# Performance work log

Hardware: AMD Instinct MI355X
Metric: run time of the kernel (lower is better)

The kernel has to match this reference:

```python
import jax, jax.numpy as jnp
import numpy as np

PATCH = 16; EMBED = 768; HEADS = 12; DHEAD = 64
DEPTH_PRE = 2; DEPTH_SHORT = 8; PRIOR = 0.2
SCALE = 1.0 / float(DHEAD) ** 0.5
LN_EPS = 1e-5


def _ln(x, g, b):
    m = jnp.mean(x, -1, keepdims=True)
    v = jnp.mean(jnp.square(x - m), -1, keepdims=True)
    return (x - m) * jax.lax.rsqrt(v + LN_EPS) * g + b


def _pos_emb(T, d):
    # pos_seq = T-1 .. 0 (descending), sinusoidal [T, d]
    pos = jnp.arange(T - 1, -1, -1, dtype=jnp.float32)
    inv_freq = 1.0 / (10000.0 ** (jnp.arange(0.0, d, 2.0, dtype=jnp.float32) / d))
    s = pos[:, None] * inv_freq[None, :]
    return jnp.concatenate([jnp.sin(s), jnp.cos(s)], axis=-1)


def _rel_shift(x):
    # Transformer-XL relative shift: pad one zero col, reshape, drop first row
    b, h, q, r = x.shape
    xp = jnp.pad(x, ((0, 0), (0, 0), (0, 0), (1, 0)))
    return xp.reshape(b, h, r + 1, q)[:, :, 1:, :].reshape(b, h, q, r)


def _layer(x, r_emb, rwb, rrb, qkv_w, qkv_b, rn_w, rn_b, o_w, o_b,
           l1g, l1b, f1w, f1b, f2w, f2b, l2g, l2b):
    T, B, D = x.shape
    heads = x @ qkv_w.T + qkv_b
    q, k, v = jnp.split(heads, 3, axis=-1)
    q = q.reshape(T, B, HEADS, DHEAD)
    k = k.reshape(T, B, HEADS, DHEAD)
    v = v.reshape(T, B, HEADS, DHEAD)
    rk = (r_emb @ rn_w.T + rn_b).reshape(T, HEADS, DHEAD)
    AC = jnp.einsum('ibnd,jbnd->bnij', q + rwb, k)
    BD = _rel_shift(jnp.einsum('ibnd,jnd->bnij', q + rrb, rk))
    prob = jax.nn.softmax(SCALE * (AC + BD), axis=-1)  # no attn_mask in this model
    av = jnp.einsum('bnij,jbnd->ibnd', prob, v).reshape(T, B, D)
    x = _ln(x + av @ o_w.T + o_b, l1g, l1b)  # post-lnorm
    h = jax.nn.gelu(x @ f1w.T + f1b, approximate=False)
    return _ln(x + h @ f2w.T + f2b, l2g, l2b)


def setup_inputs() -> dict:
    key = jax.random.key(0)
    ks = jax.random.split(key, 16)
    f = jnp.float32
    D, H, FF, L = EMBED, HEADS, 3072, DEPTH_PRE + DEPTH_SHORT

    def w(k, shape, s=0.02):
        return jax.random.normal(k, shape, dtype=f) * s

    return {
        'x': jax.random.normal(ks[0], (32, 3, 224, 224), dtype=f),
        'patch_w': w(ks[1], (D, 3, PATCH, PATCH)),
        'patch_b': jnp.zeros((D,), f),
        'r_w_bias': jnp.zeros((H, DHEAD), f),
        'r_r_bias': jnp.zeros((H, DHEAD), f),
        'qkv_w': w(ks[2], (L, 3 * D, D)),
        'qkv_b': jnp.zeros((L, 3 * D), f),
        'rnet_w': w(ks[3], (L, D, D)),
        'rnet_b': jnp.zeros((L, D), f),
        'onet_w': w(ks[4], (L, D, D)),
        'onet_b': jnp.zeros((L, D), f),
        'ln1_g': jnp.ones((L, D), f), 'ln1_b': jnp.zeros((L, D), f),
        'ff1_w': w(ks[5], (L, FF, D)),
        'ff1_b': jnp.zeros((L, FF), f),
        'ff2_w': w(ks[6], (L, D, FF)),
        'ff2_b': jnp.zeros((L, D), f),
        'ln2_g': jnp.ones((L, D), f), 'ln2_b': jnp.zeros((L, D), f),
        'null_tok': w(ks[7], (1, 1, D)),
        'down_g': jnp.ones((D,), f), 'down_b': jnp.zeros((D,), f),
        'head_w': w(ks[8], (1000, D)),
        'head_b': jnp.zeros((1000,), f),
    }


def reference(x, patch_w, patch_b, r_w_bias, r_r_bias, qkv_w, qkv_b,
              rnet_w, rnet_b, onet_w, onet_b, ln1_g, ln1_b,
              ff1_w, ff1_b, ff2_w, ff2_b, ln2_g, ln2_b,
              null_tok, down_g, down_b, head_w, head_b):
    B = x.shape[0]
    # patch embed: conv stride=kernel=PATCH, NCHW
    h = jax.lax.conv_general_dilated(
        x, patch_w, (PATCH, PATCH), 'VALID',
        dimension_numbers=('NCHW', 'OIHW', 'NCHW')) + patch_b[None, :, None, None]
    T = h.shape[2] * h.shape[3]  # 196
    h = h.reshape(B, EMBED, T).transpose(2, 0, 1)  # [T, B, D]
    r = _pos_emb(T, EMBED)

    def blk(z, i, rr):
        return _layer(z, rr, r_w_bias, r_r_bias,
                      qkv_w[i], qkv_b[i], rnet_w[i], rnet_b[i],
                      onet_w[i], onet_b[i], ln1_g[i], ln1_b[i],
                      ff1_w[i], ff1_b[i], ff2_w[i], ff2_b[i],
                      ln2_g[i], ln2_b[i])

    for i in range(DEPTH_PRE):
        h = blk(h, i, r)

    # flop_measure boundaries: 1 every interval tokens; downsample = segment mean
    interval = max(1, int(1 / PRIOR))  # 5
    bnd = (jnp.arange(T) % interval == 0).astype(h.dtype)
    seg = (jnp.cumsum(bnd) - bnd).astype(jnp.int32)  # segment id per token
    S = int(np.ceil(T / interval))  # 40 (static)
    onehot = jax.nn.one_hot(seg, S, dtype=h.dtype)  # [T, S]
    pool = onehot / jnp.sum(onehot, axis=0, keepdims=True)
    short = jnp.einsum('tbd,ts->sbd', h, pool)  # [S, B, D]
    short = jnp.concatenate(
        [jnp.broadcast_to(null_tok.reshape(1, 1, EMBED), (1, B, EMBED)), short], axis=0)
    h = _ln(short, down_g, down_b)  # [S+1, B, D]

    r2 = _pos_emb(h.shape[0], EMBED)
    for i in range(DEPTH_PRE, DEPTH_PRE + DEPTH_SHORT):
        h = blk(h, i, r2)

    return h.mean(axis=0) @ head_w.T + head_b  # [B, 1000]
```

## Files before the change

### kernel.cpp

```cpp
#include <hip/hip_runtime.h>
#include <hip/hip_bf16.h>
#include <math.h>
#include <stdint.h>

typedef __bf16 bf16;
typedef __bf16 bf16x8 __attribute__((ext_vector_type(8)));
typedef float  f32x4  __attribute__((ext_vector_type(4)));

#define NB   32
#define ED   768
#define NH   12
#define DHD  64
#define FFD  3072
#define TT1  196
#define TT2  41
#define TPM  208
#define MM1  6272
#define MM2  1408
#define M2R  1312
#define BHN  384
#define LTOT 10
#define SCL  0.125f
#define VTS  224

__device__ __forceinline__ void gload_lds16(const bf16* g, bf16* l) {
  __builtin_amdgcn_global_load_lds(
      (__attribute__((address_space(1))) void*)(uintptr_t)g,
      (__attribute__((address_space(3))) void*)(uint32_t)(uintptr_t)l,
      16, 0, 0);
}

__device__ __forceinline__ float block_sum(float v, float* red, int tid) {
#pragma unroll
  for (int o = 32; o; o >>= 1) v += __shfl_xor(v, o);
  if ((tid & 63) == 0) red[tid >> 6] = v;
  __syncthreads();
  float t = red[0] + red[1] + red[2] + red[3];
  __syncthreads();
  return t;
}

__device__ __forceinline__ float gelu_f(float v) {
  const float u = v * (0.7978845608f + 0.0356774081f * v * v);
  const float t = 1.0f - 2.0f / (__expf(2.0f * u) + 1.0f);
  return 0.5f * v * (1.0f + t);
}

__device__ __forceinline__ bf16x8 cvt8(const float* __restrict__ s) {
  const f32x4 a = *(const f32x4*)s;
  const f32x4 b = *(const f32x4*)(s + 4);
  bf16x8 o;
#pragma unroll
  for (int j = 0; j < 4; ++j) { o[j] = (bf16)a[j]; o[4 + j] = (bf16)b[j]; }
  return o;
}

__global__ void k_cvt(const float* __restrict__ s, bf16* __restrict__ d, long n8) {
  for (long i = (long)blockIdx.x * 256 + threadIdx.x; i < n8; i += (long)gridDim.x * 256)
    *(bf16x8*)&d[i * 8] = cvt8(&s[i * 8]);
}

__global__ void k_cvt4(const float* __restrict__ a, const float* __restrict__ b,
                       const float* __restrict__ c, const float* __restrict__ d,
                       bf16* __restrict__ oa, bf16* __restrict__ ob,
                       bf16* __restrict__ oc, bf16* __restrict__ od,
                       int na8, int nb8, int nc8, int nd8) {
  const long tot = (long)na8 + nb8 + nc8 + nd8;
  for (long i = (long)blockIdx.x * 256 + threadIdx.x; i < tot; i += (long)gridDim.x * 256) {
    if (i < na8) *(bf16x8*)&oa[i * 8] = cvt8(&a[i * 8]);
    else if (i < (long)na8 + nb8) { const long j = i - na8; *(bf16x8*)&ob[j * 8] = cvt8(&b[j * 8]); }
    else if (i < (long)na8 + nb8 + nc8) { const long j = i - na8 - nb8; *(bf16x8*)&oc[j * 8] = cvt8(&c[j * 8]); }
    else { const long j = i - na8 - nb8 - nc8; *(bf16x8*)&od[j * 8] = cvt8(&d[j * 8]); }
  }
}

__global__ void k_posemb(bf16* __restrict__ out, int T) {
  const int t = blockIdx.x, c = threadIdx.x;
  float v = 0.0f;
  if (t < T) {
    const float pos = (float)(T - 1 - t);
    const int ci = (c < 384) ? c : c - 384;
    const float invf = expf(-(float)ci * (9.210340371976184f / 384.0f));
    const float a = pos * invf;
    v = (c < 384) ? sinf(a) : cosf(a);
  }
  out[(long)t * ED + c] = (bf16)v;
}

__global__ void k_im2col(const float* __restrict__ x, bf16* __restrict__ A0) {
  const long idx = (long)blockIdx.x * 256 + threadIdx.x;
  if (idx >= (long)MM1 * ED) return;
  const int row = (int)(idx / ED), k = (int)(idx % ED);
  const int t = row >> 5, b = row & 31;
  const int c = k >> 8, rem = k & 255, i = rem >> 4, j = rem & 15;
  const int py = t / 14, px = t % 14;
  A0[idx] = (bf16)x[((long)(b * 3 + c) * 224 + (py * 16 + i)) * 224 + px * 16 + j];
}

template <int EPI>
__global__ __launch_bounds__(256) void k_gemm(const bf16* __restrict__ A, const bf16* __restrict__ Bw,
                                              const float* __restrict__ bias,
                                              float* __restrict__ Cf, bf16* __restrict__ Cb,
                                              int M, int N, int K, int LDK) {
  __shared__ __align__(16) bf16 As[3][128 * 32];
  __shared__ __align__(16) bf16 Bs[3][128 * 32];
  const int tid = threadIdx.x;
  const int l = tid & 63, w = tid >> 6;
  const int wr = w >> 1, wc = w & 1;
  const int m0 = blockIdx.y * 128, n0 = blockIdx.x * 128;
  const long koff = (long)blockIdx.z * K;
  const int srow = l >> 2;
  const int scol = ((l & 3) ^ ((l >> 3) & 3)) * 8;
  f32x4 acc[4][4] = {};
  const int nt = K >> 5;

  auto stage = [&](int t, int b) {
    const int kt = t << 5;
#pragma unroll
    for (int p = 0; p < 2; ++p) {
      const int rbase = w * 32 + p * 16;
      gload_lds16(&A[(long)(m0 + rbase + srow) * LDK + koff + kt + scol], &As[b][rbase * 32]);
      gload_lds16(&Bw[(long)(n0 + rbase + srow) * LDK + koff + kt + scol], &Bs[b][rbase * 32]);
    }
  };

  stage(0, 0);
  stage(1, 1);

  int cur = 0;
  for (int t = 0; t < nt; ++t) {
    if (t + 2 < nt) {
      stage(t + 2, cur == 0 ? 2 : cur - 1);
      asm volatile("s_waitcnt vmcnt(8)" ::: "memory");
    } else if (t + 1 < nt) {
      asm volatile("s_waitcnt vmcnt(4)" ::: "memory");
    } else {
      asm volatile("s_waitcnt vmcnt(0)" ::: "memory");
    }
    __builtin_amdgcn_s_barrier();
    {
      bf16x8 af[4], bg[4];
      const int ub = l >> 4;
#pragma unroll
      for (int m = 0; m < 4; ++m) {
        const int row = wr * 64 + m * 16 + (l & 15);
        af[m] = *(const bf16x8*)&As[cur][row * 32 + (ub ^ ((row >> 1) & 3)) * 8];
      }
#pragma unroll
      for (int n = 0; n < 4; ++n) {
        const int row = wc * 64 + n * 16 + (l & 15);
        bg[n] = *(const bf16x8*)&Bs[cur][row * 32 + (ub ^ ((row >> 1) & 3)) * 8];
      }
#pragma unroll
      for (int m = 0; m < 4; ++m)
#pragma unroll
        for (int n = 0; n < 4; ++n)
          acc[m][n] = __builtin_amdgcn_mfma_f32_16x16x32_bf16(af[m], bg[n], acc[m][n], 0, 0, 0);
    }
    asm volatile("s_waitcnt lgkmcnt(0)" ::: "memory");
    __builtin_amdgcn_s_barrier();
    cur = (cur == 2) ? 0 : cur + 1;
  }

  const long pbase = (EPI == 4) ? (long)blockIdx.z * M * N : 0;
#pragma unroll
  for (int m = 0; m < 4; ++m) {
    const int row = m0 + wr * 64 + m * 16 + 4 * (l >> 4);
#pragma unroll
    for (int n = 0; n < 4; ++n) {
      const int col = n0 + wc * 64 + n * 16 + (l & 15);
      const float bv = (EPI == 4) ? 0.0f : bias[col];
#pragma unroll
      for (int r = 0; r < 4; ++r) {
        const float v = acc[m][n][r] + bv;
        const long off = (long)(row + r) * N + col;
        if (EPI == 0) {
          Cf[off] = v;
        } else if (EPI == 1) {
          Cb[off] = (bf16)gelu_f(v);
        } else if (EPI == 2) {
          Cf[off] = v;
          Cb[off] = (bf16)v;
        } else if (EPI == 3) {
          Cb[off] = (bf16)v;
        } else {
          Cf[pbase + off] = v;
        }
      }
    }
  }
}

__global__ __launch_bounds__(256) void k_redk_ln(const float* __restrict__ P, const float* __restrict__ bias,
                                                 const float* __restrict__ g, const float* __restrict__ bb,
                                                 const float* __restrict__ xin,
                                                 float* __restrict__ xo, bf16* __restrict__ xbo,
                                                 int KS, long MN, int Mreal) {
  const int row = blockIdx.x, tid = threadIdx.x;
  const long base = (long)row * ED;
  __shared__ float red[4];
  if (row >= Mreal) {
#pragma unroll
    for (int e = 0; e < 3; ++e) { xo[base + tid + e * 256] = 0.0f; xbo[base + tid + e * 256] = (bf16)0.0f; }
    return;
  }
  float v[3];
#pragma unroll
  for (int e = 0; e < 3; ++e) {
    const int c = tid + e * 256;
    float a = bias[c] + xin[base + c];
    for (int ks = 0; ks < KS; ++ks) a += P[(long)ks * MN + base + c];
    v[e] = a;
  }
  const float mean = block_sum(v[0] + v[1] + v[2], red, tid) * (1.0f / ED);
  float sq = 0.0f;
#pragma unroll
  for (int e = 0; e < 3; ++e) { const float dd = v[e] - mean; sq += dd * dd; }
  const float var = block_sum(sq, red, tid) * (1.0f / ED);
  const float rs = rsqrtf(var + 1e-5f);
#pragma unroll
  for (int e = 0; e < 3; ++e) {
    const int c = tid + e * 256;
    const float o = (v[e] - mean) * rs * g[c] + bb[c];
    xo[base + c] = o;
    xbo[base + c] = (bf16)o;
  }
}

__global__ __launch_bounds__(256) void k_vrepack(const bf16* __restrict__ heads, bf16* __restrict__ vT) {
  const int bh = blockIdx.x;
  const int b = bh / NH, n = bh % NH;
  const int tid = threadIdx.x;
  __shared__ __align__(16) bf16 vTl[64 * 232];
  for (int task = tid; task < 224 * 8; task += 256) {
    const int j = task >> 3, c8 = (task & 7) * 8;
    bf16x8 vv = {};
    if (j < TT1) vv = *(const bf16x8*)&heads[((long)(j * NB + b)) * (3 * ED) + 2 * ED + n * 64 + c8];
#pragma unroll
    for (int e = 0; e < 8; ++e) {
      const int d = c8 + e;
      vTl[d * 232 + (j ^ (((d >> 3) & 3) << 3))] = vv[e];
    }
  }
  __syncthreads();
  bf16* dst = vT + (long)bh * 64 * VTS;
  for (int task = tid; task < 64 * 28; task += 256) {
    const int d = task / 28, u = task % 28;
    const int j0 = u * 8;
    const int x = ((d >> 3) & 3) << 3;
    *(bf16x8*)&dst[d * VTS + j0] = *(const bf16x8*)&vTl[d * 232 + (j0 ^ x)];
  }
}

__global__ __launch_bounds__(256) void k_attn_pre(
    const bf16* __restrict__ heads, const float* __restrict__ rwb, const float* __restrict__ rrb,
    const bf16* __restrict__ rkb_l, const bf16* __restrict__ vT, bf16* __restrict__ avb) {
  const int r0 = blockIdx.x * 32;
  const int bh = blockIdx.y;
  const int b = bh / NH, n = bh % NH;
  const int tid = threadIdx.x;
  const int l = tid & 63, w = tid >> 6;
  const int fr = l & 15;
  const int fc = 8 * (l >> 4);
  __shared__ float Sl[32 * 209];
  __shared__ __align__(16) bf16 probl[32 * 232];
  __shared__ float red8[256];
  __shared__ float rstat[32];

  {
    const int ti = w & 1;
    const int ar = r0 + ti * 16 + fr;
    bf16x8 qa0 = {}, qa1 = {};
    if (ar < TT1) {
      const bf16* qp = &heads[((long)(ar * NB + b)) * (3 * ED) + n * 64];
      qa0 = *(const bf16x8*)(qp + fc);
      qa1 = *(const bf16x8*)(qp + 32 + fc);
    }
    bf16x8 q0, q1;
#pragma unroll
    for (int e = 0; e < 8; ++e) {
      q0[e] = (bf16)((float)qa0[e] + rwb[n * 64 + fc + e]);
      q1[e] = (bf16)((float)qa1[e] + rwb[n * 64 + 32 + fc + e]);
    }
    auto ldk = [&](int tj, bf16x8& k0, bf16x8& k1) {
      const int br = tj * 16 + fr;
      k0 = bf16x8{}; k1 = bf16x8{};
      if (br < TT1) {
        const bf16* kp = &heads[((long)(br * NB + b)) * (3 * ED) + ED + n * 64];
        k0 = *(const bf16x8*)(kp + fc);
        k1 = *(const bf16x8*)(kp + 32 + fc);
      }
    };
    bf16x8 k0, k1, nk0, nk1;
    const int tj0 = w >> 1;
    ldk(tj0, k0, k1);
    for (int tj = tj0; tj < 13; tj += 2) {
      if (tj + 2 < 13) ldk(tj + 2, nk0, nk1);
      f32x4 c = {};
      c = __builtin_amdgcn_mfma_f32_16x16x32_bf16(q0, k0, c, 0, 0, 0);
      c = __builtin_amdgcn_mfma_f32_16x16x32_bf16(q1, k1, c, 0, 0, 0);
      const int scol = tj * 16 + fr;
      const int srb = ti * 16 + 4 * (l >> 4);
#pragma unroll
      for (int r = 0; r < 4; ++r) Sl[(srb + r) * 209 + scol] = SCL * c[r];
      k0 = nk0; k1 = nk1;
    }
  }
  __syncthreads();

  {
    bf16x8 qr0[3], qr1[3];
#pragma unroll
    for (int ta = 0; ta < 3; ++ta) {
      const int ar = r0 + ta * 16 + fr;
      bf16x8 qa0 = {}, qa1 = {};
      if (ar < TT1) {
        const bf16* qp = &heads[((long)(ar * NB + b)) * (3 * ED) + n * 64];
        qa0 = *(const bf16x8*)(qp + fc);
        qa1 = *(const bf16x8*)(qp + 32 + fc);
      }
#pragma unroll
      for (int e = 0; e < 8; ++e) {
        qr0[ta][e] = (bf16)((float)qa0[e] + rrb[n * 64 + fc + e]);
        qr1[ta][e] = (bf16)((float)qa1[e] + rrb[n * 64 + 32 + fc + e]);
      }
    }
    auto ldr = [&](int tb, bf16x8& g0, bf16x8& g1) {
      const int br = tb * 16 + fr;
      const bf16* rp = &rkb_l[((long)n * TPM + br) * 64];
      g0 = *(const bf16x8*)(rp + fc);
      g1 = *(const bf16x8*)(rp + 32 + fc);
    };
    bf16x8 g0, g1, ng0, ng1;
    if (w < 13) ldr(w, g0, g1);
    for (int tb = w; tb < 13; tb += 4) {
      if (tb + 4 < 13) ldr(tb + 4, ng0, ng1);
#pragma unroll
      for (int ta = 0; ta < 3; ++ta) {
        f32x4 c = {};
        c = __builtin_amdgcn_mfma_f32_16x16x32_bf16(qr0[ta], g0, c, 0, 0, 0);
        c = __builtin_amdgcn_mfma_f32_16x16x32_bf16(qr1[ta], g1, c, 0, 0, 0);
        const int bcol = tb * 16 + fr;
        const int ab = r0 + ta * 16 + 4 * (l >> 4);
#pragma unroll
        for (int r = 0; r < 4; ++r) {
          const int a = ab + r;
          if (a < TT1 && bcol < TT1) {
            const int m = a * (TT1 + 1) + bcol + 1;
            if (m >= TT1) {
              const int i = m / TT1 - 1;
              const int j = m - (i + 1) * TT1;
              const int li = i - r0;
              if (li >= 0 && li < 32) Sl[li * 209 + j] += SCL * c[r];
            }
          }
        }
      }
      g0 = ng0; g1 = ng1;
    }
  }
  __syncthreads();

  const int sr = tid & 31, sg = tid >> 5;
  const bool rowok = (r0 + sr) < TT1;
  const int j0 = sg * 25;
  const int j1 = (j0 + 25 < TT1) ? j0 + 25 : TT1;
  float pm = -3.0e38f;
  if (rowok) {
    for (int j = j0; j < j1; ++j) pm = fmaxf(pm, Sl[sr * 209 + j]);
  }
  red8[sr * 8 + sg] = pm;
  __syncthreads();
  if (tid < 32) {
    float m0 = red8[tid * 8];
#pragma unroll
    for (int q = 1; q < 8; ++q) m0 = fmaxf(m0, red8[tid * 8 + q]);
    rstat[tid] = m0;
  }
  __syncthreads();
  const float rm = rstat[sr];
  float ps = 0.0f;
  if (rowok) {
    for (int j = j0; j < j1; ++j) {
      const float e = __expf(Sl[sr * 209 + j] - rm);
      Sl[sr * 209 + j] = e;
      ps += e;
    }
  }
  red8[sr * 8 + sg] = ps;
  __syncthreads();
  if (tid < 32) {
    float s0 = 0.0f;
#pragma unroll
    for (int q = 0; q < 8; ++q) s0 += red8[tid * 8 + q];
    rstat[tid] = (s0 > 0.0f) ? 1.0f / s0 : 0.0f;
  }
  __syncthreads();
  const float inv = rstat[sr];
  const int sx = ((sr >> 3) & 3) << 3;
  for (int j = sg * 28; j < sg * 28 + 28; ++j) {
    const float v = (rowok && j < TT1) ? Sl[sr * 209 + j] * inv : 0.0f;
    probl[sr * 232 + (j ^ sx)] = (bf16)v;
  }
  __syncthreads();

  const bf16* vTg = vT + (long)bh * 64 * VTS;
  for (int tt = w; tt < 8; tt += 4) {
    const int ti = tt & 1, dj = tt >> 1;
    const int prow = ti * 16 + fr;
    const int vrow = dj * 16 + fr;
    const int px = ((prow >> 3) & 3) << 3;
    f32x4 c = {};
#pragma unroll
    for (int kk = 0; kk < 224; kk += 32) {
      const int j0v = kk + fc;
      const bf16x8 pa = *(const bf16x8*)&probl[prow * 232 + (j0v ^ px)];
      const bf16x8 vb = *(const bf16x8*)&vTg[vrow * VTS + j0v];
      c = __builtin_amdgcn_mfma_f32_16x16x32_bf16(pa, vb, c, 0, 0, 0);
    }
    const int d = dj * 16 + fr;
    const int ib = ti * 16 + 4 * (l >> 4);
#pragma unroll
    for (int r = 0; r < 4; ++r) {
      const int gi = r0 + ib + r;
      if (gi < TT1) avb[((long)(gi * NB + b)) * ED + n * 64 + d] = (bf16)c[r];
    }
  }
}

__global__ __launch_bounds__(256) void k_attn_short(
    const bf16* __restrict__ heads, const float* __restrict__ rwb, const float* __restrict__ rrb,
    const bf16* __restrict__ rkb_l, bf16* __restrict__ avb) {
  const int bh = blockIdx.x;
  const int b = bh / NH, n = bh % NH;
  const int tid = threadIdx.x;
  const int l = tid & 63, w = tid >> 6;
  const int fr = l & 15, fc = 8 * (l >> 4);
  __shared__ float Sl[48 * 49];
  __shared__ __align__(16) bf16 probl[48 * 72];
  __shared__ __align__(16) bf16 vTl[64 * 72];

  for (int task = tid; task < 64 * 8; task += 256) {
    const int j = task >> 3, c8 = (task & 7) * 8;
    bf16x8 vv = {};
    if (j < TT2) vv = *(const bf16x8*)&heads[((long)(j * NB + b)) * (3 * ED) + 2 * ED + n * 64 + c8];
#pragma unroll
    for (int e = 0; e < 8; ++e) {
      const int d = c8 + e;
      vTl[d * 72 + (j ^ (((d >> 3) & 3) << 3))] = vv[e];
    }
  }

  for (int tt = w; tt < 9; tt += 4) {
    const int ti = tt / 3, tj = tt % 3;
    const int ar = ti * 16 + fr;
    const int br = tj * 16 + fr;
    f32x4 c = {};
#pragma unroll
    for (int kk = 0; kk < 64; kk += 32) {
      const int col = kk + fc;
      bf16x8 qa = {}, kb = {};
      if (ar < 44) qa = *(const bf16x8*)&heads[((long)(ar * NB + b)) * (3 * ED) + n * 64 + col];
      if (br < 44) kb = *(const bf16x8*)&heads[((long)(br * NB + b)) * (3 * ED) + ED + n * 64 + col];
      bf16x8 qq;
#pragma unroll
      for (int e = 0; e < 8; ++e) qq[e] = (bf16)((float)qa[e] + rwb[n * 64 + col + e]);
      c = __builtin_amdgcn_mfma_f32_16x16x32_bf16(qq, kb, c, 0, 0, 0);
    }
    const int scol = tj * 16 + fr;
    const int srb = ti * 16 + 4 * (l >> 4);
#pragma unroll
    for (int r = 0; r < 4; ++r) Sl[(srb + r) * 49 + scol] = SCL * c[r];
  }
  __syncthreads();

  for (int tt = w; tt < 9; tt += 4) {
    const int ti = tt / 3, tj = tt % 3;
    const int ar = ti * 16 + fr;
    const int br = tj * 16 + fr;
    f32x4 c = {};
#pragma unroll
    for (int kk = 0; kk < 64; kk += 32) {
      const int col = kk + fc;
      bf16x8 qa = {};
      if (ar < 44) qa = *(const bf16x8*)&heads[((long)(ar * NB + b)) * (3 * ED) + n * 64 + col];
      const bf16x8 rk = *(const bf16x8*)&rkb_l[((long)n * TPM + br) * 64 + col];
      bf16x8 qq;
#pragma unroll
      for (int e = 0; e < 8; ++e) qq[e] = (bf16)((float)qa[e] + rrb[n * 64 + col + e]);
      c = __builtin_amdgcn_mfma_f32_16x16x32_bf16(qq, rk, c, 0, 0, 0);
    }
    const int bcol = tj * 16 + fr;
    const int ab = ti * 16 + 4 * (l >> 4);
#pragma unroll
    for (int r = 0; r < 4; ++r) {
      const int a = ab + r;
      if (a < TT2 && bcol < TT2) {
        const int m = a * (TT2 + 1) + bcol + 1;
        if (m >= TT2) {
          const int i = m / TT2 - 1;
          const int j = m - (i + 1) * TT2;
          Sl[i * 49 + j] += SCL * c[r];
        }
      }
    }
  }
  __syncthreads();

  if (tid < 48) {
    const int i = tid;
    const int ix = ((i >> 3) & 3) << 3;
    if (i < TT2) {
      float mx = -3.0e38f;
      for (int j = 0; j < TT2; ++j) mx = fmaxf(mx, Sl[i * 49 + j]);
      float sm = 0.0f;
      for (int j = 0; j < TT2; ++j) { const float e = expf(Sl[i * 49 + j] - mx); Sl[i * 49 + j] = e; sm += e; }
      const float inv = 1.0f / sm;
      for (int j = 0; j < TT2; ++j) probl[i * 72 + (j ^ ix)] = (bf16)(Sl[i * 49 + j] * inv);
      for (int j = TT2; j < 64; ++j) probl[i * 72 + (j ^ ix)] = (bf16)0.0f;
    } else {
      for (int j = 0; j < 64; ++j) probl[i * 72 + (j ^ ix)] = (bf16)0.0f;
    }
  }
  __syncthreads();

  for (int tt = w; tt < 12; tt += 4) {
    const int ti = tt % 3, dj = tt / 3;
    const int prow = ti * 16 + fr;
    const int vrow = dj * 16 + fr;
    const int px = ((prow >> 3) & 3) << 3;
    const int vx = ((vrow >> 3) & 3) << 3;
    f32x4 c = {};
#pragma unroll
    for (int kk = 0; kk < 64; kk += 32) {
      const int j0 = kk + fc;
      const bf16x8 pa = *(const bf16x8*)&probl[prow * 72 + (j0 ^ px)];
      const bf16x8 vb = *(const bf16x8*)&vTl[vrow * 72 + (j0 ^ vx)];
      c = __builtin_amdgcn_mfma_f32_16x16x32_bf16(pa, vb, c, 0, 0, 0);
    }
    const int d = dj * 16 + fr;
    const int ib = ti * 16 + 4 * (l >> 4);
#pragma unroll
    for (int r = 0; r < 4; ++r) {
      const int i = ib + r;
      if (i < TT2) avb[((long)(i * NB + b)) * ED + n * 64 + d] = (bf16)c[r];
    }
  }
}

__global__ void k_rkrepack(const float* __restrict__ rkall, bf16* __restrict__ rkb,
                           int T, int Ncols, int l0) {
  const int i = blockIdx.x, z = blockIdx.y, d = threadIdx.x;
  const float v = (i < T) ? rkall[(long)i * Ncols + z * ED + d] : 0.0f;
  const int n = d >> 6, dh = d & 63;
  rkb[(((long)(l0 + z) * NH + n) * TPM + i) * 64 + dh] = (bf16)v;
}

__global__ __launch_bounds__(256) void k_ln(const float* __restrict__ xin, const float* __restrict__ add,
                                            const float* __restrict__ g, const float* __restrict__ bb,
                                            float* __restrict__ xo, bf16* __restrict__ xbo, int Mreal) {
  const int row = blockIdx.x, tid = threadIdx.x;
  const long base = (long)row * ED;
  __shared__ float red[4];
  if (row >= Mreal) {
#pragma unroll
    for (int e = 0; e < 3; ++e) { xo[base + tid + e * 256] = 0.0f; xbo[base + tid + e * 256] = (bf16)0.0f; }
    return;
  }
  float v[3];
#pragma unroll
  for (int e = 0; e < 3; ++e) v[e] = xin[base + tid + e * 256] + add[base + tid + e * 256];
  const float mean = block_sum(v[0] + v[1] + v[2], red, tid) * (1.0f / ED);
  float sq = 0.0f;
#pragma unroll
  for (int e = 0; e < 3; ++e) { const float dd = v[e] - mean; sq += dd * dd; }
  const float var = block_sum(sq, red, tid) * (1.0f / ED);
  const float rs = rsqrtf(var + 1e-5f);
#pragma unroll
  for (int e = 0; e < 3; ++e) {
    const int c = tid + e * 256;
    const float o = (v[e] - mean) * rs * g[c] + bb[c];
    xo[base + c] = o;
    xbo[base + c] = (bf16)o;
  }
}

__global__ __launch_bounds__(256) void k_down(const float* __restrict__ x, const float* __restrict__ nullt,
                                              const float* __restrict__ g, const float* __restrict__ bb,
                                              float* __restrict__ xo, bf16* __restrict__ xbo) {
  const int row = blockIdx.x, tid = threadIdx.x;
  const long base = (long)row * ED;
  __shared__ float red[4];
  if (row >= TT2 * NB) {
#pragma unroll
    for (int e = 0; e < 3; ++e) { xo[base + tid + e * 256] = 0.0f; xbo[base + tid + e * 256] = (bf16)0.0f; }
    return;
  }
  const int s = row >> 5, b = row & 31;
  float v[3];
  if (s == 0) {
#pragma unroll
    for (int e = 0; e < 3; ++e) v[e] = nullt[tid + e * 256];
  } else {
    const int seg = s - 1;
    const int t0 = (seg == 0) ? 0 : (5 * seg - 4);
    const int cnt = (seg == 0) ? 1 : 5;
#pragma unroll
    for (int e = 0; e < 3; ++e) {
      float a = 0.0f;
      for (int tt = 0; tt < cnt; ++tt) a += x[((long)((t0 + tt) * NB + b)) * ED + tid + e * 256];
      v[e] = a / (float)cnt;
    }
  }
  const float mean = block_sum(v[0] + v[1] + v[2], red, tid) * (1.0f / ED);
  float sq = 0.0f;
#pragma unroll
  for (int e = 0; e < 3; ++e) { const float dd = v[e] - mean; sq += dd * dd; }
  const float var = block_sum(sq, red, tid) * (1.0f / ED);
  const float rs = rsqrtf(var + 1e-5f);
#pragma unroll
  for (int e = 0; e < 3; ++e) {
    const int c = tid + e * 256;
    const float o = (v[e] - mean) * rs * g[c] + bb[c];
    xo[base + c] = o;
    xbo[base + c] = (bf16)o;
  }
}

__global__ __launch_bounds__(256) void k_mean(const float* __restrict__ x2, float* __restrict__ xm) {
  const int b = blockIdx.x, tid = threadIdx.x;
#pragma unroll
  for (int e = 0; e < 3; ++e) {
    const int c = tid + e * 256;
    float a = 0.0f;
    for (int s = 0; s < TT2; ++s) a += x2[((long)(s * NB + b)) * ED + c];
    xm[(long)b * ED + c] = a * (1.0f / TT2);
  }
}

__global__ __launch_bounds__(256) void k_head(const float* __restrict__ xm, const float* __restrict__ hw,
                                              const float* __restrict__ hbias, float* __restrict__ out) {
  const int gid = blockIdx.x * 4 + (threadIdx.x >> 6);
  const int l = threadIdx.x & 63;
  if (gid >= NB * 1000) return;
  const int b = gid / 1000, n = gid % 1000;
  const float* xr = xm + (long)b * ED;
  const float* wr = hw + (long)n * ED;
  float a = 0.0f;
#pragma unroll
  for (int e = 0; e < 12; ++e) a += xr[l + 64 * e] * wr[l + 64 * e];
#pragma unroll
  for (int o = 32; o; o >>= 1) a += __shfl_xor(a, o);
  if (l == 0) out[(long)b * 1000 + n] = a + hbias[n];
}

extern "C" void kernel_launch(void* const* d_in, const int* in_sizes, int n_in,
                              void* d_out, int out_size, void* d_ws, size_t ws_size,
                              hipStream_t stream) {
  const float* in_x     = (const float*)d_in[0];
  const float* patch_w  = (const float*)d_in[1];
  const float* patch_b  = (const float*)d_in[2];
  const float* r_w_bias = (const float*)d_in[3];
  const float* r_r_bias = (const float*)d_in[4];
  const float* qkv_w    = (const float*)d_in[5];
  const float* qkv_b    = (const float*)d_in[6];
  const float* rnet_w   = (const float*)d_in[7];
  const float* rnet_b   = (const float*)d_in[8];
  const float* onet_w   = (const float*)d_in[9];
  const float* onet_b   = (const float*)d_in[10];
  const float* ln1_g    = (const float*)d_in[11];
  const float* ln1_b    = (const float*)d_in[12];
  const float* ff1_w    = (const float*)d_in[13];
  const float* ff1_b    = (const float*)d_in[14];
  const float* ff2_w    = (const float*)d_in[15];
  const float* ff2_b    = (const float*)d_in[16];
  const float* ln2_g    = (const float*)d_in[17];
  const float* ln2_b    = (const float*)d_in[18];
  const float* null_tok = (const float*)d_in[19];
  const float* down_g   = (const float*)d_in[20];
  const float* down_b   = (const float*)d_in[21];
  const float* head_w   = (const float*)d_in[22];
  const float* head_b   = (const float*)d_in[23];
  float* out = (float*)d_out;

  char* base = (char*)d_ws;
  size_t off = 0;
  auto take = [&](size_t bytes) -> char* {
    char* r = base + off;
    off += (bytes + 255) & ~(size_t)255;
    return r;
  };

  float* x    = (float*)take((size_t)MM1 * ED * 4);
  bf16*  xb   = (bf16*)take((size_t)MM1 * ED * 2);
  float* x2   = (float*)take((size_t)MM2 * ED * 4);
  bf16*  xb2  = (bf16*)take((size_t)MM2 * ED * 2);
  bf16*  rkb  = (bf16*)take((size_t)LTOT * NH * TPM * 64 * 2);
  bf16*  rbf  = (bf16*)take((size_t)256 * ED * 2);
  bf16*  r2bf = (bf16*)take((size_t)128 * ED * 2);
  float* xm   = (float*)take((size_t)NB * ED * 4);

  char* arenaW = take((size_t)(2304 * 768 + 768 * 768 + 3072 * 768 + 768 * 3072) * 2);
  bf16* wq = (bf16*)arenaW;
  bf16* wo = wq + (size_t)2304 * 768;
  bf16* w1 = wo + (size_t)768 * 768;
  bf16* w2 = w1 + (size_t)3072 * 768;
  bf16* wrnet  = (bf16*)arenaW;
  bf16* wpatch = wrnet + (size_t)LTOT * 768 * 768;

  char* arenaQ = take((size_t)MM1 * ED * 2 + (size_t)4 * MM2 * ED * 4);
  bf16*  A0 = (bf16*)arenaQ;
  bf16*  vT = (bf16*)arenaQ;
  float* P  = (float*)arenaQ;

  char* arenaH = take((size_t)MM1 * 3 * ED * 2);
  bf16*  headsb = (bf16*)arenaH;
  float* rkall1 = (float*)arenaH;
  float* rkall2 = (float*)(arenaH + (size_t)256 * 1536 * 4);

  char* arenaS = take((size_t)MM1 * ED * 2 + (size_t)MM1 * ED * 4 + (size_t)MM1 * FFD * 2);
  bf16*  avb  = (bf16*)arenaS;
  float* gout = (float*)(arenaS + (size_t)MM1 * ED * 2);
  bf16*  hb   = (bf16*)(arenaS + (size_t)MM1 * ED * 2 + (size_t)MM1 * ED * 4);

  if (off > ws_size) return;

  k_posemb<<<dim3(256), dim3(768), 0, stream>>>(rbf, TT1);
  k_posemb<<<dim3(128), dim3(768), 0, stream>>>(r2bf, TT2);
  k_cvt<<<dim3(1024), dim3(256), 0, stream>>>(rnet_w, wrnet, (long)LTOT * 768 * 768 / 8);
  k_cvt<<<dim3(288), dim3(256), 0, stream>>>(patch_w, wpatch, (long)768 * 768 / 8);
  k_im2col<<<dim3((MM1 * ED + 255) / 256), dim3(256), 0, stream>>>(in_x, A0);
  k_gemm<2><<<dim3(6, 49, 1), dim3(256), 0, stream>>>(A0, wpatch, patch_b, x, xb, MM1, ED, ED, ED);
  k_gemm<0><<<dim3(12, 2, 1), dim3(256), 0, stream>>>(rbf, wrnet, rnet_b, rkall1, nullptr, 256, 1536, ED, ED);
  k_gemm<0><<<dim3(48, 1, 1), dim3(256), 0, stream>>>(r2bf, wrnet + (size_t)2 * 768 * 768, rnet_b + 2 * 768,
                                                      rkall2, nullptr, 128, 6144, ED, ED);
  k_rkrepack<<<dim3(TPM, 2), dim3(768), 0, stream>>>(rkall1, rkb, TT1, 1536, 0);
  k_rkrepack<<<dim3(48, 8), dim3(768), 0, stream>>>(rkall2, rkb, TT2, 6144, 2);

  for (int l = 0; l < LTOT; ++l) {
    const bool pre = (l < 2);
    const int Mp = pre ? MM1 : MM2;
    const int Mreal = pre ? MM1 : M2R;
    float* xcur = pre ? x : x2;
    bf16* xbcur = pre ? xb : xb2;

    k_cvt4<<<dim3(1024), dim3(256), 0, stream>>>(
        qkv_w + (size_t)l * 2304 * 768, onet_w + (size_t)l * 768 * 768,
        ff1_w + (size_t)l * 3072 * 768, ff2_w + (size_t)l * 768 * 3072,
        wq, wo, w1, w2, 2304 * 768 / 8, 768 * 768 / 8, 3072 * 768 / 8, 768 * 3072 / 8);

    k_gemm<3><<<dim3(18, Mp / 128, 1), dim3(256), 0, stream>>>(xbcur, wq, qkv_b + (size_t)l * 2304,
                                                               nullptr, headsb, Mp, 3 * ED, ED, ED);
    if (pre) {
      k_vrepack<<<dim3(BHN), dim3(256), 0, stream>>>(headsb, vT);
      k_attn_pre<<<dim3(7, BHN), dim3(256), 0, stream>>>(
          headsb, r_w_bias, r_r_bias, rkb + (size_t)l * NH * TPM * 64, vT, avb);
      k_gemm<0><<<dim3(6, Mp / 128, 1), dim3(256), 0, stream>>>(avb, wo, onet_b + (size_t)l * 768,
                                                                gout, nullptr, Mp, ED, ED, ED);
      k_ln<<<dim3(Mp), dim3(256), 0, stream>>>(xcur, gout, ln1_g + (size_t)l * 768, ln1_b + (size_t)l * 768,
                                               xcur, xbcur, Mreal);
      k_gemm<1><<<dim3(24, Mp / 128, 1), dim3(256), 0, stream>>>(xbcur, w1, ff1_b + (size_t)l * 3072,
                                                                 nullptr, hb, Mp, FFD, ED, ED);
      k_gemm<0><<<dim3(6, Mp / 128, 1), dim3(256), 0, stream>>>(hb, w2, ff2_b + (size_t)l * 768,
                                                                gout, nullptr, Mp, ED, FFD, FFD);
      k_ln<<<dim3(Mp), dim3(256), 0, stream>>>(xcur, gout, ln2_g + (size_t)l * 768, ln2_b + (size_t)l * 768,
                                               xcur, xbcur, Mreal);
    } else {
      k_attn_short<<<dim3(BHN), dim3(256), 0, stream>>>(
          headsb, r_w_bias, r_r_bias, rkb + (size_t)l * NH * TPM * 64, avb);
      k_gemm<4><<<dim3(6, Mp / 128, 2), dim3(256), 0, stream>>>(avb, wo, nullptr,
                                                                P, nullptr, Mp, ED, 384, ED);
      k_redk_ln<<<dim3(Mp), dim3(256), 0, stream>>>(P, onet_b + (size_t)l * 768,
                                                    ln1_g + (size_t)l * 768, ln1_b + (size_t)l * 768,
                                                    xcur, xcur, xbcur, 2, (long)Mp * ED, Mreal);
      k_gemm<1><<<dim3(24, Mp / 128, 1), dim3(256), 0, stream>>>(xbcur, w1, ff1_b + (size_t)l * 3072,
                                                                 nullptr, hb, Mp, FFD, ED, ED);
      k_gemm<4><<<dim3(6, Mp / 128, 4), dim3(256), 0, stream>>>(hb, w2, nullptr,
                                                                P, nullptr, Mp, ED, 768, FFD);
      k_redk_ln<<<dim3(Mp), dim3(256), 0, stream>>>(P, ff2_b + (size_t)l * 768,
                                                    ln2_g + (size_t)l * 768, ln2_b + (size_t)l * 768,
                                                    xcur, xcur, xbcur, 4, (long)Mp * ED, Mreal);
    }

    if (l == 1) {
      k_down<<<dim3(MM2), dim3(256), 0, stream>>>(x, null_tok, down_g, down_b, x2, xb2);
    }
  }

  k_mean<<<dim3(NB), dim3(256), 0, stream>>>(x2, xm);
  k_head<<<dim3(8000), dim3(256), 0, stream>>>(xm, head_w, head_b, out);
}
```

Measured before the change: 1.447 ms.

## Read fp32 weights directly in short-stage GEMMs, remap blocks across XCDs

For the eight short-sequence layers, the GEMM now streams fp32 weights straight into LDS and converts them to bf16 at fragment-load time. This removes the per-layer k_cvt4 conversion kernel, along with its extra write and re-read of the weights. The cost is twice the weight bytes per tile, larger LDS use, and conversion ALU work in the inner loop. All GEMMs also get a block-index remap so that consecutive tiles land on the same XCD, which is meant to improve L2 locality.

```diff
diff --git a/kernel.cpp b/kernel.cpp
--- a/kernel.cpp
+++ b/kernel.cpp
@@ -23,7 +23,7 @@
 #define SCL  0.125f
 #define VTS  224
 
-__device__ __forceinline__ void gload_lds16(const bf16* g, bf16* l) {
+__device__ __forceinline__ void gload_lds16(const void* g, void* l) {
   __builtin_amdgcn_global_load_lds(
       (__attribute__((address_space(1))) void*)(uintptr_t)g,
       (__attribute__((address_space(3))) void*)(uint32_t)(uintptr_t)l,
@@ -97,20 +97,34 @@
   A0[idx] = (bf16)x[((long)(b * 3 + c) * 224 + (py * 16 + i)) * 224 + px * 16 + j];
 }
 
-template <int EPI>
+template <int EPI, int BF32>
 __global__ __launch_bounds__(256) void k_gemm(const bf16* __restrict__ A, const bf16* __restrict__ Bw,
+                                              const float* __restrict__ Bw32,
                                               const float* __restrict__ bias,
                                               float* __restrict__ Cf, bf16* __restrict__ Cb,
                                               int M, int N, int K, int LDK) {
-  __shared__ __align__(16) bf16 As[3][128 * 32];
-  __shared__ __align__(16) bf16 Bs[3][128 * 32];
+  constexpr int BELEM = 128 * 32;
+  __shared__ __align__(16) bf16 As[3][BELEM];
+  constexpr int BBYTES = BF32 ? 3 * BELEM * 4 : 3 * BELEM * 2;
+  __shared__ __align__(16) char Braw[BBYTES];
   const int tid = threadIdx.x;
   const int l = tid & 63, w = tid >> 6;
   const int wr = w >> 1, wc = w & 1;
-  const int m0 = blockIdx.y * 128, n0 = blockIdx.x * 128;
+
+  const int gx = gridDim.x, gy = gridDim.y;
+  int flat = blockIdx.x * gy + blockIdx.y;
+  const int nwg = gx * gy;
+  const int xcd = flat & 7, idx = flat >> 3;
+  const int qq = nwg >> 3, rr = nwg & 7;
+  flat = (xcd < rr ? xcd * (qq + 1) : rr * (qq + 1) + (xcd - rr) * qq) + idx;
+  const int bx = flat / gy;
+  const int m0 = (flat - bx * gy) * 128, n0 = bx * 128;
+
   const long koff = (long)blockIdx.z * K;
-  const int srow = l >> 2;
-  const int scol = ((l & 3) ^ ((l >> 3) & 3)) * 8;
+  const int srowA = l >> 2;
+  const int scolA = ((l & 3) ^ ((l >> 3) & 3)) * 8;
+  const int srowB = l >> 3;
+  const int scolB = ((l & 7) ^ (((l >> 3) & 3) << 1)) * 4;
   f32x4 acc[4][4] = {};
   const int nt = K >> 5;
 
@@ -119,8 +133,22 @@
 #pragma unroll
     for (int p = 0; p < 2; ++p) {
       const int rbase = w * 32 + p * 16;
-      gload_lds16(&A[(long)(m0 + rbase + srow) * LDK + koff + kt + scol], &As[b][rbase * 32]);
-      gload_lds16(&Bw[(long)(n0 + rbase + srow) * LDK + koff + kt + scol], &Bs[b][rbase * 32]);
+      gload_lds16(&A[(long)(m0 + rbase + srowA) * LDK + koff + kt + scolA], &As[b][rbase * 32]);
+    }
+    if constexpr (BF32) {
+      float* Bb = (float*)Braw + (long)b * BELEM;
+#pragma unroll
+      for (int p = 0; p < 4; ++p) {
+        const int rbase = w * 32 + p * 8;
+        gload_lds16(&Bw32[(long)(n0 + rbase + srowB) * LDK + koff + kt + scolB], &Bb[rbase * 32]);
+      }
+    } else {
+      bf16* Bb = (bf16*)Braw + (long)b * BELEM;
+#pragma unroll
+      for (int p = 0; p < 2; ++p) {
+        const int rbase = w * 32 + p * 16;
+        gload_lds16(&Bw[(long)(n0 + rbase + srowA) * LDK + koff + kt + scolA], &Bb[rbase * 32]);
+      }
     }
   };
 
@@ -131,9 +159,11 @@
   for (int t = 0; t < nt; ++t) {
     if (t + 2 < nt) {
       stage(t + 2, cur == 0 ? 2 : cur - 1);
-      asm volatile("s_waitcnt vmcnt(8)" ::: "memory");
+      if constexpr (BF32) asm volatile("s_waitcnt vmcnt(12)" ::: "memory");
+      else                asm volatile("s_waitcnt vmcnt(8)" ::: "memory");
     } else if (t + 1 < nt) {
-      asm volatile("s_waitcnt vmcnt(4)" ::: "memory");
+      if constexpr (BF32) asm volatile("s_waitcnt vmcnt(6)" ::: "memory");
+      else                asm volatile("s_waitcnt vmcnt(4)" ::: "memory");
     } else {
       asm volatile("s_waitcnt vmcnt(0)" ::: "memory");
     }
@@ -146,10 +176,25 @@
         const int row = wr * 64 + m * 16 + (l & 15);
         af[m] = *(const bf16x8*)&As[cur][row * 32 + (ub ^ ((row >> 1) & 3)) * 8];
       }
-#pragma unroll
-      for (int n = 0; n < 4; ++n) {
-        const int row = wc * 64 + n * 16 + (l & 15);
-        bg[n] = *(const bf16x8*)&Bs[cur][row * 32 + (ub ^ ((row >> 1) & 3)) * 8];
+      if constexpr (BF32) {
+        const float* Bb = (const float*)Braw + (long)cur * BELEM;
+        const int u0 = ub << 1;
+#pragma unroll
+        for (int n = 0; n < 4; ++n) {
+          const int row = wc * 64 + n * 16 + (l & 15);
+          const int slot0 = u0 ^ ((row & 3) << 1);
+          const f32x4 lo = *(const f32x4*)&Bb[row * 32 + slot0 * 4];
+          const f32x4 hi = *(const f32x4*)&Bb[row * 32 + slot0 * 4 + 4];
+#pragma unroll
+          for (int j = 0; j < 4; ++j) { bg[n][j] = (bf16)lo[j]; bg[n][4 + j] = (bf16)hi[j]; }
+        }
+      } else {
+        const bf16* Bb = (const bf16*)Braw + (long)cur * BELEM;
+#pragma unroll
+        for (int n = 0; n < 4; ++n) {
+          const int row = wc * 64 + n * 16 + (l & 15);
+          bg[n] = *(const bf16x8*)&Bb[row * 32 + (ub ^ ((row >> 1) & 3)) * 8];
+        }
       }
 #pragma unroll
       for (int m = 0; m < 4; ++m)
@@ -730,10 +775,11 @@
   k_cvt<<<dim3(1024), dim3(256), 0, stream>>>(rnet_w, wrnet, (long)LTOT * 768 * 768 / 8);
   k_cvt<<<dim3(288), dim3(256), 0, stream>>>(patch_w, wpatch, (long)768 * 768 / 8);
   k_im2col<<<dim3((MM1 * ED + 255) / 256), dim3(256), 0, stream>>>(in_x, A0);
-  k_gemm<2><<<dim3(6, 49, 1), dim3(256), 0, stream>>>(A0, wpatch, patch_b, x, xb, MM1, ED, ED, ED);
-  k_gemm<0><<<dim3(12, 2, 1), dim3(256), 0, stream>>>(rbf, wrnet, rnet_b, rkall1, nullptr, 256, 1536, ED, ED);
-  k_gemm<0><<<dim3(48, 1, 1), dim3(256), 0, stream>>>(r2bf, wrnet + (size_t)2 * 768 * 768, rnet_b + 2 * 768,
-                                                      rkall2, nullptr, 128, 6144, ED, ED);
+  k_gemm<2, 0><<<dim3(6, 49, 1), dim3(256), 0, stream>>>(A0, wpatch, nullptr, patch_b, x, xb, MM1, ED, ED, ED);
+  k_gemm<0, 0><<<dim3(12, 2, 1), dim3(256), 0, stream>>>(rbf, wrnet, nullptr, rnet_b, rkall1, nullptr,
+                                                         256, 1536, ED, ED);
+  k_gemm<0, 0><<<dim3(48, 1, 1), dim3(256), 0, stream>>>(r2bf, wrnet + (size_t)2 * 768 * 768, nullptr,
+                                                         rnet_b + 2 * 768, rkall2, nullptr, 128, 6144, ED, ED);
   k_rkrepack<<<dim3(TPM, 2), dim3(768), 0, stream>>>(rkall1, rkb, TT1, 1536, 0);
   k_rkrepack<<<dim3(48, 8), dim3(768), 0, stream>>>(rkall2, rkb, TT2, 6144, 2);
 
@@ -744,39 +790,43 @@
     float* xcur = pre ? x : x2;
     bf16* xbcur = pre ? xb : xb2;
 
-    k_cvt4<<<dim3(1024), dim3(256), 0, stream>>>(
-        qkv_w + (size_t)l * 2304 * 768, onet_w + (size_t)l * 768 * 768,
-        ff1_w + (size_t)l * 3072 * 768, ff2_w + (size_t)l * 768 * 3072,
-        wq, wo, w1, w2, 2304 * 768 / 8, 768 * 768 / 8, 3072 * 768 / 8, 768 * 3072 / 8);
-
-    k_gemm<3><<<dim3(18, Mp / 128, 1), dim3(256), 0, stream>>>(xbcur, wq, qkv_b + (size_t)l * 2304,
-                                                               nullptr, headsb, Mp, 3 * ED, ED, ED);
     if (pre) {
+      k_cvt4<<<dim3(1024), dim3(256), 0, stream>>>(
+          qkv_w + (size_t)l * 2304 * 768, onet_w + (size_t)l * 768 * 768,
+          ff1_w + (size_t)l * 3072 * 768, ff2_w + (size_t)l * 768 * 3072,
+          wq, wo, w1, w2, 2304 * 768 / 8, 768 * 768 / 8, 3072 * 768 / 8, 768 * 3072 / 8);
+
+      k_gemm<3, 0><<<dim3(18, Mp / 128, 1), dim3(256), 0, stream>>>(
+          xbcur, wq, nullptr, qkv_b + (size_t)l * 2304, nullptr, headsb, Mp, 3 * ED, ED, ED);
       k_vrepack<<<dim3(BHN), dim3(256), 0, stream>>>(headsb, vT);
       k_attn_pre<<<dim3(7, BHN), dim3(256), 0, stream>>>(
           headsb, r_w_bias, r_r_bias, rkb + (size_t)l * NH * TPM * 64, vT, avb);
-      k_gemm<0><<<dim3(6, Mp / 128, 1), dim3(256), 0, stream>>>(avb, wo, onet_b + (size_t)l * 768,
-                                                                gout, nullptr, Mp, ED, ED, ED);
+      k_gemm<0, 0><<<dim3(6, Mp / 128, 1), dim3(256), 0, stream>>>(
+          avb, wo, nullptr, onet_b + (size_t)l * 768, gout, nullptr, Mp, ED, ED, ED);
       k_ln<<<dim3(Mp), dim3(256), 0, stream>>>(xcur, gout, ln1_g + (size_t)l * 768, ln1_b + (size_t)l * 768,
                                                xcur, xbcur, Mreal);
-      k_gemm<1><<<dim3(24, Mp / 128, 1), dim3(256), 0, stream>>>(xbcur, w1, ff1_b + (size_t)l * 3072,
-                                                                 nullptr, hb, Mp, FFD, ED, ED);
-      k_gemm<0><<<dim3(6, Mp / 128, 1), dim3(256), 0, stream>>>(hb, w2, ff2_b + (size_t)l * 768,
-                                                                gout, nullptr, Mp, ED, FFD, FFD);
+      k_gemm<1, 0><<<dim3(24, Mp / 128, 1), dim3(256), 0, stream>>>(
+          xbcur, w1, nullptr, ff1_b + (size_t)l * 3072, nullptr, hb, Mp, FFD, ED, ED);
+      k_gemm<0, 0><<<dim3(6, Mp / 128, 1), dim3(256), 0, stream>>>(
+          hb, w2, nullptr, ff2_b + (size_t)l * 768, gout, nullptr, Mp, ED, FFD, FFD);
       k_ln<<<dim3(Mp), dim3(256), 0, stream>>>(xcur, gout, ln2_g + (size_t)l * 768, ln2_b + (size_t)l * 768,
                                                xcur, xbcur, Mreal);
     } else {
+      k_gemm<3, 1><<<dim3(18, Mp / 128, 1), dim3(256), 0, stream>>>(
+          xbcur, nullptr, qkv_w + (size_t)l * 2304 * 768, qkv_b + (size_t)l * 2304,
+          nullptr, headsb, Mp, 3 * ED, ED, ED);
       k_attn_short<<<dim3(BHN), dim3(256), 0, stream>>>(
           headsb, r_w_bias, r_r_bias, rkb + (size_t)l * NH * TPM * 64, avb);
-      k_gemm<4><<<dim3(6, Mp / 128, 2), dim3(256), 0, stream>>>(avb, wo, nullptr,
-                                                                P, nullptr, Mp, ED, 384, ED);
+      k_gemm<4, 1><<<dim3(6, Mp / 128, 2), dim3(256), 0, stream>>>(
+          avb, nullptr, onet_w + (size_t)l * 768 * 768, nullptr, P, nullptr, Mp, ED, 384, ED);
       k_redk_ln<<<dim3(Mp), dim3(256), 0, stream>>>(P, onet_b + (size_t)l * 768,
                                                     ln1_g + (size_t)l * 768, ln1_b + (size_t)l * 768,
                                                     xcur, xcur, xbcur, 2, (long)Mp * ED, Mreal);
-      k_gemm<1><<<dim3(24, Mp / 128, 1), dim3(256), 0, stream>>>(xbcur, w1, ff1_b + (size_t)l * 3072,
-                                                                 nullptr, hb, Mp, FFD, ED, ED);
-      k_gemm<4><<<dim3(6, Mp / 128, 4), dim3(256), 0, stream>>>(hb, w2, nullptr,
-                                                                P, nullptr, Mp, ED, 768, FFD);
+      k_gemm<1, 1><<<dim3(24, Mp / 128, 1), dim3(256), 0, stream>>>(
+          xbcur, nullptr, ff1_w + (size_t)l * 3072 * 768, ff1_b + (size_t)l * 3072,
+          nullptr, hb, Mp, FFD, ED, ED);
+      k_gemm<4, 1><<<dim3(6, Mp / 128, 4), dim3(256), 0, stream>>>(
+          hb, nullptr, ff2_w + (size_t)l * 768 * 3072, nullptr, P, nullptr, Mp, ED, 768, FFD);
       k_redk_ln<<<dim3(Mp), dim3(256), 0, stream>>>(P, ff2_b + (size_t)l * 768,
                                                     ln2_g + (size_t)l * 768, ln2_b + (size_t)l * 768,
                                                     xcur, xcur, xbcur, 4, (long)Mp * ED, Mreal);
```

Measured after the change: 1.524 ms. 5.3% more time.
